# Performance work log

Hardware: AMD Instinct MI355X
Metric: run time of the kernel (lower is better)

The kernel has to match this reference:

```python
import jax, jax.numpy as jnp
import numpy as np

N_NODES = 100000
N_EDGES = 1600000
IN_CH = 128
OUT_CH = 64
HID = 2 * OUT_CH


def setup_inputs() -> dict:
    key = jax.random.key(0)
    ks = jax.random.split(key, 9)
    x = jax.random.normal(ks[0], (N_NODES, IN_CH), dtype=jnp.float32)
    edge_index = jax.random.randint(ks[1], (2, N_EDGES), 0, N_NODES, dtype=jnp.int64)
    s = 0.05
    W1 = jax.random.normal(ks[2], (IN_CH, HID), dtype=jnp.float32) * s
    b1 = jnp.zeros((HID,), dtype=jnp.float32)
    Wmu = jax.random.normal(ks[3], (HID, OUT_CH), dtype=jnp.float32) * s
    bmu = jnp.zeros((OUT_CH,), dtype=jnp.float32)
    Wls = jax.random.normal(ks[4], (HID, OUT_CH), dtype=jnp.float32) * s
    bls = jnp.zeros((OUT_CH,), dtype=jnp.float32)
    eps = jax.random.normal(ks[5], (N_NODES, OUT_CH), dtype=jnp.float32)
    return {"x": x, "edge_index": edge_index, "W1": W1, "b1": b1,
            "Wmu": Wmu, "bmu": bmu, "Wls": Wls, "bls": bls, "eps": eps}


def _gcn_conv(x, W, b, src, dst, dis):
    # PyG GCNConv: out = D^{-1/2}(A+I)D^{-1/2} X W + b, self-loops added.
    h = x @ W  # [N, F]
    norm = dis[src] * dis[dst]  # per-edge symmetric norm
    msg = h[src] * norm[:, None]  # [E, F] gathered + scaled messages
    agg = jax.ops.segment_sum(msg, dst, num_segments=x.shape[0])
    agg = agg + h * (dis * dis)[:, None]  # self-loop term
    return agg + b


def reference(x, edge_index, W1, b1, Wmu, bmu, Wls, bls, eps):
    src, dst = edge_index[0], edge_index[1]
    N = x.shape[0]
    # degree over A + I (aggregation at dst, +1 for self loop)
    deg = jax.ops.segment_sum(jnp.ones_like(dst, dtype=x.dtype), dst,
                              num_segments=N) + 1.0
    dis = jax.lax.rsqrt(deg)  # deg >= 1, safe
    h = _gcn_conv(x, W1, b1, src, dst, dis)
    mu = _gcn_conv(h, Wmu, bmu, src, dst, dis)
    logstd = _gcn_conv(h, Wls, bls, src, dst, dis)
    z = mu + eps * jnp.exp(logstd)  # reparametrization trick
    return (z, mu, logstd)
```

## Files before the change

kernel.cpp:

```cpp
#include <hip/hip_runtime.h>
#include <hip/hip_bf16.h>


typedef unsigned int u32;
typedef unsigned short u16;
typedef unsigned char u8;
typedef __bf16 bf16x8 __attribute__((ext_vector_type(8)));
typedef float f32x4 __attribute__((ext_vector_type(4)));

__device__ __forceinline__ u16 f2bf(float f) {
    union { float f; u32 u; } v; v.f = f;
    u32 u = v.u;
    u += 0x7fffu + ((u >> 16) & 1u);
    return (u16)(u >> 16);
}
__device__ __forceinline__ float bflo(u32 p) {
    union { u32 u; float f; } v; v.u = p << 16; return v.f;
}
__device__ __forceinline__ float bfhi(u32 p) {
    union { u32 u; float f; } v; v.u = p & 0xffff0000u; return v.f;
}

__global__ __launch_bounds__(256) void deg_hist(const int* __restrict__ dst,
                                                u32* __restrict__ deg,
                                                u8* __restrict__ loc, int E) {
    int i4 = (blockIdx.x * 256 + threadIdx.x) * 4;
    if (i4 + 3 < E) {
        int4 d4 = *(const int4*)(dst + i4);
        uchar4 l4;
        l4.x = (u8)atomicAdd(&deg[d4.x], 1u);
        l4.y = (u8)atomicAdd(&deg[d4.y], 1u);
        l4.z = (u8)atomicAdd(&deg[d4.z], 1u);
        l4.w = (u8)atomicAdd(&deg[d4.w], 1u);
        *(uchar4*)(loc + i4) = l4;
    } else {
        for (int i = i4; i < E; ++i) loc[i] = (u8)atomicAdd(&deg[dst[i]], 1u);
    }
}

__global__ __launch_bounds__(256) void scanA(const u32* __restrict__ deg,
                                             u32* __restrict__ blockSums, int N) {
    __shared__ u32 s[256];
    int t = threadIdx.x, i = blockIdx.x * 256 + t;
    s[t] = (i < N) ? deg[i] : 0u;
    for (int off = 128; off > 0; off >>= 1) {
        __syncthreads();
        if (t < off) s[t] += s[t + off];
    }
    if (t == 0) blockSums[blockIdx.x] = s[0];
}

__global__ __launch_bounds__(512) void scanB(const u32* __restrict__ blockSums,
                                             u32* __restrict__ blockOffs, int NB) {
    __shared__ u32 s[512];
    int t = threadIdx.x;
    u32 v = (t < NB) ? blockSums[t] : 0u;
    s[t] = v;
    for (int off = 1; off < 512; off <<= 1) {
        __syncthreads();
        u32 add = (t >= off) ? s[t - off] : 0u;
        __syncthreads();
        s[t] += add;
    }
    __syncthreads();
    if (t < NB) blockOffs[t] = s[t] - v;
}

__global__ __launch_bounds__(256) void scanC(const u32* __restrict__ deg,
                                             const u32* __restrict__ blockOffs,
                                             u32* __restrict__ rowstart,
                                             float* __restrict__ dis, int N, int E) {
    __shared__ u32 s[256];
    int t = threadIdx.x, i = blockIdx.x * 256 + t;
    u32 v = (i < N) ? deg[i] : 0u;
    s[t] = v;
    for (int off = 1; off < 256; off <<= 1) {
        __syncthreads();
        u32 add = (t >= off) ? s[t - off] : 0u;
        __syncthreads();
        s[t] += add;
    }
    __syncthreads();
    if (i < N) {
        rowstart[i] = blockOffs[blockIdx.x] + s[t] - v;
        dis[i] = rsqrtf((float)v + 1.0f);
    }
    if (i == 0) rowstart[N] = (u32)E;
}

__global__ __launch_bounds__(256) void place_kernel(const int* __restrict__ src,
                                                    const int* __restrict__ dst,
                                                    const u8* __restrict__ loc,
                                                    const u32* __restrict__ rowstart,
                                                    int* __restrict__ csr, int E) {
    int i4 = (blockIdx.x * 256 + threadIdx.x) * 4;
    if (i4 + 3 < E) {
        int4 s4 = *(const int4*)(src + i4);
        int4 d4 = *(const int4*)(dst + i4);
        uchar4 l4 = *(const uchar4*)(loc + i4);
        csr[rowstart[d4.x] + l4.x] = s4.x;
        csr[rowstart[d4.y] + l4.y] = s4.y;
        csr[rowstart[d4.z] + l4.z] = s4.z;
        csr[rowstart[d4.w] + l4.w] = s4.w;
    } else {
        for (int i = i4; i < E; ++i) csr[rowstart[dst[i]] + loc[i]] = src[i];
    }
}

__global__ __launch_bounds__(256) void fuse_w(const float* __restrict__ W1,
                                              const float* __restrict__ Wmu,
                                              const float* __restrict__ Wls,
                                              const float* __restrict__ b1,
                                              const float* __restrict__ bmu,
                                              const float* __restrict__ bls,
                                              u16* __restrict__ WfT,
                                              float* __restrict__ bb,
                                              float* __restrict__ bcat) {
    int idx = blockIdx.x * 256 + threadIdx.x;
    if (idx >= 16384) return;
    int k = idx >> 7, n = idx & 127;
    const float* Wcol = (n < 64) ? (Wmu + n) : (Wls + (n - 64));
    float acc = 0.f;
#pragma unroll 8
    for (int j = 0; j < 128; ++j) acc += W1[k * 128 + j] * Wcol[j * 64];
    WfT[n * 128 + k] = f2bf(acc);
    if (k == 0) {
        float accb = 0.f;
#pragma unroll 8
        for (int j = 0; j < 128; ++j) accb += b1[j] * Wcol[j * 64];
        bb[n] = accb;
        bcat[n] = (n < 64) ? bmu[n] : bls[n - 64];
    }
}

__global__ __launch_bounds__(256) void convert_x(const float* __restrict__ x,
                                                 const float* __restrict__ dis,
                                                 u32* __restrict__ xs,
                                                 u32* __restrict__ ts, int N) {
    long i = (long)blockIdx.x * 256 + threadIdx.x;
    long node = i >> 5;
    if (node > N) return;
    if (node == N) {
        ((uint2*)xs)[i] = make_uint2(0u, 0u);
        ((uint2*)ts)[i] = make_uint2(0u, 0u);
        return;
    }
    float dd = dis[node];
    f32x4 v = ((const f32x4*)x)[i];
    u32 p0 = (u32)f2bf(v[0] * dd) | ((u32)f2bf(v[1] * dd) << 16);
    u32 p1 = (u32)f2bf(v[2] * dd) | ((u32)f2bf(v[3] * dd) << 16);
    ((uint2*)xs)[i] = make_uint2(p0, p1);
}

__global__ __launch_bounds__(256) void g1gemm(const u32* __restrict__ xs,
                                              const int* __restrict__ csr,
                                              const u32* __restrict__ rowstart,
                                              const float* __restrict__ dis,
                                              const u16* __restrict__ WfT,
                                              const float* __restrict__ bb,
                                              u16* __restrict__ ts, int N) {
    __shared__ __align__(16) u16 ytile[16][136];
    __shared__ float disS[16];
    int tid = threadIdx.x, blk = blockIdx.x;
    int wave = tid >> 6, lane = tid & 63;
    int sub = lane >> 4, l = lane & 15;
    int nl = wave * 4 + sub;
    int node = blk * 16 + nl;
    bool live = node < N;
    int nodeC = live ? node : 0;
    float dd = dis[nodeC];
    u32 beg = live ? rowstart[nodeC] : 0u;
    u32 end = live ? rowstart[nodeC + 1] : 0u;
    if (tid < 16) disS[tid] = (blk * 16 + tid < N) ? dis[blk * 16 + tid] : 0.f;

    const uint4* xs4 = (const uint4*)xs;
    uint4 selfv = xs4[(long)nodeC * 16 + l];
    float a0 = bflo(selfv.x), a1 = bfhi(selfv.x);
    float a2 = bflo(selfv.y), a3 = bfhi(selfv.y);
    float a4 = bflo(selfv.z), a5 = bfhi(selfv.z);
    float a6 = bflo(selfv.w), a7 = bfhi(selfv.w);

    int s = (beg + (u32)l < end) ? csr[beg + l] : N;
    for (u32 e0 = beg; e0 < end; e0 += 16) {
        u32 e1 = e0 + 16;
        int sn = (e1 < end && e1 + (u32)l < end) ? csr[e1 + l] : N;
#pragma unroll
        for (int h = 0; h < 2; ++h) {
            int sj[8]; uint4 w[8];
#pragma unroll
            for (int j = 0; j < 8; ++j) sj[j] = __shfl(s, sub * 16 + h * 8 + j);
#pragma unroll
            for (int j = 0; j < 8; ++j) w[j] = xs4[(long)sj[j] * 16 + l];
#pragma unroll
            for (int j = 0; j < 8; ++j) {
                a0 += bflo(w[j].x); a1 += bfhi(w[j].x);
                a2 += bflo(w[j].y); a3 += bfhi(w[j].y);
                a4 += bflo(w[j].z); a5 += bfhi(w[j].z);
                a6 += bflo(w[j].w); a7 += bfhi(w[j].w);
            }
        }
        s = sn;
    }
    uint4 o = make_uint4(0u, 0u, 0u, 0u);
    if (live) {
        o.x = (u32)f2bf(a0 * dd) | ((u32)f2bf(a1 * dd) << 16);
        o.y = (u32)f2bf(a2 * dd) | ((u32)f2bf(a3 * dd) << 16);
        o.z = (u32)f2bf(a4 * dd) | ((u32)f2bf(a5 * dd) << 16);
        o.w = (u32)f2bf(a6 * dd) | ((u32)f2bf(a7 * dd) << 16);
    }
    *(uint4*)&ytile[nl][l * 8] = o;
    __syncthreads();

    int quad = sub, mn = l;
    bf16x8 af[4];
#pragma unroll
    for (int kk = 0; kk < 4; ++kk)
        af[kk] = *reinterpret_cast<const bf16x8*>(&ytile[mn][kk * 32 + quad * 8]);

#pragma unroll
    for (int n0 = 0; n0 < 2; ++n0) {
        int col = wave * 32 + n0 * 16 + mn;
        f32x4 acc = {0.f, 0.f, 0.f, 0.f};
#pragma unroll
        for (int kk = 0; kk < 4; ++kk) {
            bf16x8 bf =
                *reinterpret_cast<const bf16x8*>(&WfT[col * 128 + kk * 32 + quad * 8]);
            acc = __builtin_amdgcn_mfma_f32_16x16x32_bf16(af[kk], bf, acc, 0, 0, 0);
        }
        float bc = bb[col];
#pragma unroll
        for (int r = 0; r < 4; ++r) {
            int row = quad * 4 + r;
            int gn = blk * 16 + row;
            if (gn < N) ts[(long)gn * 128 + col] = f2bf((acc[r] + bc) * disS[row]);
        }
    }
}

__global__ __launch_bounds__(256) void gather2(const u32* __restrict__ ts,
                                               const int* __restrict__ csr,
                                               const u32* __restrict__ rowstart,
                                               const float* __restrict__ dis,
                                               const float* __restrict__ bcat,
                                               const float* __restrict__ eps,
                                               float* __restrict__ out, int N) {
    int wid = (blockIdx.x * 256 + threadIdx.x) >> 6;
    int sub = (threadIdx.x & 63) >> 4, l = threadIdx.x & 15;
    int node = wid * 4 + sub;
    bool live = node < N;
    int nodeC = live ? node : 0;
    float dd = dis[nodeC];
    u32 beg = live ? rowstart[nodeC] : 0u;
    u32 end = live ? rowstart[nodeC + 1] : 0u;
    const uint4* ts4 = (const uint4*)ts;

    uint4 selfv = ts4[(long)nodeC * 16 + l];
    float a0 = bflo(selfv.x), a1 = bfhi(selfv.x);
    float a2 = bflo(selfv.y), a3 = bfhi(selfv.y);
    float a4 = bflo(selfv.z), a5 = bfhi(selfv.z);
    float a6 = bflo(selfv.w), a7 = bfhi(selfv.w);

    int s = (beg + (u32)l < end) ? csr[beg + l] : N;
    for (u32 e0 = beg; e0 < end; e0 += 16) {
        u32 e1 = e0 + 16;
        int sn = (e1 < end && e1 + (u32)l < end) ? csr[e1 + l] : N;
#pragma unroll
        for (int h = 0; h < 2; ++h) {
            int sj[8]; uint4 w[8];
#pragma unroll
            for (int j = 0; j < 8; ++j) sj[j] = __shfl(s, sub * 16 + h * 8 + j);
#pragma unroll
            for (int j = 0; j < 8; ++j) w[j] = ts4[(long)sj[j] * 16 + l];
#pragma unroll
            for (int j = 0; j < 8; ++j) {
                a0 += bflo(w[j].x); a1 += bfhi(w[j].x);
                a2 += bflo(w[j].y); a3 += bfhi(w[j].y);
                a4 += bflo(w[j].z); a5 += bfhi(w[j].z);
                a6 += bflo(w[j].w); a7 += bfhi(w[j].w);
            }
        }
        s = sn;
    }

    int c0 = l * 8;
    f32x4 clo = ((const f32x4*)bcat)[2 * l], chi = ((const f32x4*)bcat)[2 * l + 1];
    float v0 = a0 * dd + clo[0];
    float v1 = a1 * dd + clo[1];
    float v2 = a2 * dd + clo[2];
    float v3 = a3 * dd + clo[3];
    float v4 = a4 * dd + chi[0];
    float v5 = a5 * dd + chi[1];
    float v6 = a6 * dd + chi[2];
    float v7 = a7 * dd + chi[3];

    int srcl = (threadIdx.x & 63) + 8;
    float w0 = __shfl(v0, srcl), w1 = __shfl(v1, srcl), w2 = __shfl(v2, srcl),
          w3 = __shfl(v3, srcl), w4 = __shfl(v4, srcl), w5 = __shfl(v5, srcl),
          w6 = __shfl(v6, srcl), w7 = __shfl(v7, srcl);

    if (!live) return;
    long NO = (long)N * 64;
    if (l < 8) {
        float* mu = out + NO + (long)node * 64 + c0;
        ((f32x4*)mu)[0] = f32x4{v0, v1, v2, v3};
        ((f32x4*)mu)[1] = f32x4{v4, v5, v6, v7};
        const float* ep = eps + (long)node * 64 + c0;
        f32x4 e0v = ((const f32x4*)ep)[0], e1v = ((const f32x4*)ep)[1];
        float* z = out + (long)node * 64 + c0;
        ((f32x4*)z)[0] = f32x4{v0 + e0v[0] * __expf(w0), v1 + e0v[1] * __expf(w1),
                               v2 + e0v[2] * __expf(w2), v3 + e0v[3] * __expf(w3)};
        ((f32x4*)z)[1] = f32x4{v4 + e1v[0] * __expf(w4), v5 + e1v[1] * __expf(w5),
                               v6 + e1v[2] * __expf(w6), v7 + e1v[3] * __expf(w7)};
    } else {
        float* ls = out + 2 * NO + (long)node * 64 + (c0 - 64);
        ((f32x4*)ls)[0] = f32x4{v0, v1, v2, v3};
        ((f32x4*)ls)[1] = f32x4{v4, v5, v6, v7};
    }
}

extern "C" void kernel_launch(void* const* d_in, const int* in_sizes, int n_in,
                              void* d_out, int out_size, void* d_ws, size_t ws_size,
                              hipStream_t stream) {
    const float* x   = (const float*)d_in[0];
    const int* ei    = (const int*)d_in[1];
    const float* W1  = (const float*)d_in[2];
    const float* b1  = (const float*)d_in[3];
    const float* Wmu = (const float*)d_in[4];
    const float* bmu = (const float*)d_in[5];
    const float* Wls = (const float*)d_in[6];
    const float* bls = (const float*)d_in[7];
    const float* eps = (const float*)d_in[8];
    float* out = (float*)d_out;

    const int N = in_sizes[0] / 128;
    const int E = in_sizes[1] / 2;
    const int* src = ei;
    const int* dst = ei + E;
    const int NB = (N + 255) / 256;

    char* ws = (char*)d_ws;
    u32* deg       = (u32*)(ws + 0);
    u32* rowstart  = (u32*)(ws + 401408);
    u32* blockSums = (u32*)(ws + 802816);
    u32* blockOffs = (u32*)(ws + 804864);
    float* dis     = (float*)(ws + 806912);
    u16* WfT       = (u16*)(ws + 1208320);
    float* bb      = (float*)(ws + 1241088);
    float* bcat    = (float*)(ws + 1241600);
    u8* loc        = (u8*)(ws + 1242112);
    int* csr       = (int*)(ws + 2842112);
    u32* xs        = (u32*)(ws + 9242112);
    u32* ts        = (u32*)(ws + 34842368);

    hipMemsetAsync(deg, 0, 400000, stream);

    int gridE4 = (E / 4 + 255) / 256;
    deg_hist<<<gridE4, 256, 0, stream>>>(dst, deg, loc, E);
    scanA<<<NB, 256, 0, stream>>>(deg, blockSums, N);
    scanB<<<1, 512, 0, stream>>>(blockSums, blockOffs, NB);
    scanC<<<NB, 256, 0, stream>>>(deg, blockOffs, rowstart, dis, N, E);
    place_kernel<<<gridE4, 256, 0, stream>>>(src, dst, loc, rowstart, csr, E);
    fuse_w<<<64, 256, 0, stream>>>(W1, Wmu, Wls, b1, bmu, bls, WfT, bb, bcat);

    long Qc = (long)(N + 1) * 32;
    convert_x<<<(int)((Qc + 255) / 256), 256, 0, stream>>>(x, dis, xs, ts, N);

    int gridT = (N + 15) / 16;
    g1gemm<<<gridT, 256, 0, stream>>>(xs, csr, rowstart, dis, WfT, bb,
                                      (u16*)ts, N);

    int gridG = ((N + 3) / 4 * 64 + 255) / 256;
    gather2<<<gridG, 256, 0, stream>>>(ts, csr, rowstart, dis, bcat, eps, out, N);
}
```

Measured before the change: 422.7 us.

## Slice feature tables into column panels and split gather from GEMM

The bf16 feature tables are stored as 8 column slices of 32 bytes per node. Each block now gathers one slice, so the random-access working set per slice is small enough to stay in cache. The fused gather+GEMM kernel is split into a separate gather pass that writes y and a standalone MFMA GEMM that writes the sliced layout, with non-temporal loads and stores for streaming data. The cost is an extra kernel launch, an extra round trip of y through memory, more redundant csr index reads (one per slice), and narrower per-lane gathers.

```diff
diff --git a/kernel.cpp b/kernel.cpp
--- a/kernel.cpp
+++ b/kernel.cpp
@@ -7,6 +7,8 @@
 typedef unsigned char u8;
 typedef __bf16 bf16x8 __attribute__((ext_vector_type(8)));
 typedef float f32x4 __attribute__((ext_vector_type(4)));
+typedef u32 u32x2 __attribute__((ext_vector_type(2)));
+typedef u32 u32x4 __attribute__((ext_vector_type(4)));
 
 __device__ __forceinline__ u16 f2bf(float f) {
     union { float f; u32 u; } v; v.f = f;
@@ -135,83 +137,124 @@
 
 __global__ __launch_bounds__(256) void convert_x(const float* __restrict__ x,
                                                  const float* __restrict__ dis,
-                                                 u32* __restrict__ xs,
-                                                 u32* __restrict__ ts, int N) {
+                                                 u32* __restrict__ xsP, int N) {
     long i = (long)blockIdx.x * 256 + threadIdx.x;
     long node = i >> 5;
+    int j = (int)(i & 31);
     if (node > N) return;
+    int s = j >> 2, q = j & 3;
+    u32x2* dst = (u32x2*)((char*)xsP + ((size_t)s * (N + 1) + node) * 32 + q * 8);
     if (node == N) {
-        ((uint2*)xs)[i] = make_uint2(0u, 0u);
-        ((uint2*)ts)[i] = make_uint2(0u, 0u);
+        u32x2 z = {0u, 0u};
+        __builtin_nontemporal_store(z, dst);
         return;
     }
     float dd = dis[node];
     f32x4 v = ((const f32x4*)x)[i];
-    u32 p0 = (u32)f2bf(v[0] * dd) | ((u32)f2bf(v[1] * dd) << 16);
-    u32 p1 = (u32)f2bf(v[2] * dd) | ((u32)f2bf(v[3] * dd) << 16);
-    ((uint2*)xs)[i] = make_uint2(p0, p1);
-}
-
-__global__ __launch_bounds__(256) void g1gemm(const u32* __restrict__ xs,
-                                              const int* __restrict__ csr,
-                                              const u32* __restrict__ rowstart,
-                                              const float* __restrict__ dis,
-                                              const u16* __restrict__ WfT,
-                                              const float* __restrict__ bb,
-                                              u16* __restrict__ ts, int N) {
-    __shared__ __align__(16) u16 ytile[16][136];
-    __shared__ float disS[16];
-    int tid = threadIdx.x, blk = blockIdx.x;
-    int wave = tid >> 6, lane = tid & 63;
-    int sub = lane >> 4, l = lane & 15;
-    int nl = wave * 4 + sub;
-    int node = blk * 16 + nl;
+    u32x2 o;
+    o.x = (u32)f2bf(v[0] * dd) | ((u32)f2bf(v[1] * dd) << 16);
+    o.y = (u32)f2bf(v[2] * dd) | ((u32)f2bf(v[3] * dd) << 16);
+    __builtin_nontemporal_store(o, dst);
+}
+
+#define GATHER_SLICE()                                                          \
+    int pairbase = (tid & 63) & ~1;                                             \
+    int id[8];                                                                  \
+    u32 e0 = beg;                                                               \
+    if (e0 < end) {                                                             \
+        _Pragma("unroll")                                                       \
+        for (int k = 0; k < 4; ++k) {                                           \
+            u32 q0 = e0 + p * 4 + k, q1 = e0 + 8 + p * 4 + k;                   \
+            id[k]     = (q0 < end) ? __builtin_nontemporal_load(csr + q0) : N;  \
+            id[4 + k] = (q1 < end) ? __builtin_nontemporal_load(csr + q1) : N;  \
+        }                                                                       \
+    }                                                                           \
+    for (; e0 < end;) {                                                         \
+        u32 e1 = e0 + 16;                                                       \
+        int idn[8];                                                             \
+        if (e1 < end) {                                                         \
+            _Pragma("unroll")                                                   \
+            for (int k = 0; k < 4; ++k) {                                       \
+                u32 q0 = e1 + p * 4 + k, q1 = e1 + 8 + p * 4 + k;               \
+                idn[k]     = (q0 < end) ? __builtin_nontemporal_load(csr + q0) : N; \
+                idn[4 + k] = (q1 < end) ? __builtin_nontemporal_load(csr + q1) : N; \
+            }                                                                   \
+        }                                                                       \
+        _Pragma("unroll")                                                       \
+        for (int h = 0; h < 2; ++h) {                                           \
+            int sj[8]; uint4 w[8];                                              \
+            _Pragma("unroll")                                                   \
+            for (int j = 0; j < 8; ++j)                                         \
+                sj[j] = __shfl(id[h * 4 + (j & 3)], pairbase + (j >> 2));       \
+            _Pragma("unroll")                                                   \
+            for (int j = 0; j < 8; ++j) w[j] = base[(size_t)sj[j] * 2];         \
+            _Pragma("unroll")                                                   \
+            for (int j = 0; j < 8; ++j) {                                       \
+                a0 += bflo(w[j].x); a1 += bfhi(w[j].x);                         \
+                a2 += bflo(w[j].y); a3 += bfhi(w[j].y);                         \
+                a4 += bflo(w[j].z); a5 += bfhi(w[j].z);                         \
+                a6 += bflo(w[j].w); a7 += bfhi(w[j].w);                         \
+            }                                                                   \
+        }                                                                       \
+        _Pragma("unroll")                                                       \
+        for (int k = 0; k < 8; ++k) id[k] = idn[k];                             \
+        e0 = e1;                                                                \
+    }
+
+__global__ __launch_bounds__(256) void gatherY(const u32* __restrict__ xsP,
+                                               const int* __restrict__ csr,
+                                               const u32* __restrict__ rowstart,
+                                               const float* __restrict__ dis,
+                                               u16* __restrict__ y, int N) {
+    int tid = threadIdx.x;
+    u32 bid = blockIdx.x;
+    int s = bid & 7;
+    int p = tid & 1;
+    int node = (int)(bid >> 3) * 128 + (tid >> 1);
     bool live = node < N;
     int nodeC = live ? node : 0;
     float dd = dis[nodeC];
-    u32 beg = live ? rowstart[nodeC] : 0u;
-    u32 end = live ? rowstart[nodeC + 1] : 0u;
-    if (tid < 16) disS[tid] = (blk * 16 + tid < N) ? dis[blk * 16 + tid] : 0.f;
-
-    const uint4* xs4 = (const uint4*)xs;
-    uint4 selfv = xs4[(long)nodeC * 16 + l];
+    u32 beg = rowstart[nodeC];
+    u32 end = live ? rowstart[nodeC + 1] : beg;
+    const uint4* base = (const uint4*)(xsP + (size_t)s * (N + 1) * 8) + p;
+
+    uint4 selfv = base[(size_t)nodeC * 2];
     float a0 = bflo(selfv.x), a1 = bfhi(selfv.x);
     float a2 = bflo(selfv.y), a3 = bfhi(selfv.y);
     float a4 = bflo(selfv.z), a5 = bfhi(selfv.z);
     float a6 = bflo(selfv.w), a7 = bfhi(selfv.w);
 
-    int s = (beg + (u32)l < end) ? csr[beg + l] : N;
-    for (u32 e0 = beg; e0 < end; e0 += 16) {
-        u32 e1 = e0 + 16;
-        int sn = (e1 < end && e1 + (u32)l < end) ? csr[e1 + l] : N;
-#pragma unroll
-        for (int h = 0; h < 2; ++h) {
-            int sj[8]; uint4 w[8];
-#pragma unroll
-            for (int j = 0; j < 8; ++j) sj[j] = __shfl(s, sub * 16 + h * 8 + j);
-#pragma unroll
-            for (int j = 0; j < 8; ++j) w[j] = xs4[(long)sj[j] * 16 + l];
-#pragma unroll
-            for (int j = 0; j < 8; ++j) {
-                a0 += bflo(w[j].x); a1 += bfhi(w[j].x);
-                a2 += bflo(w[j].y); a3 += bfhi(w[j].y);
-                a4 += bflo(w[j].z); a5 += bfhi(w[j].z);
-                a6 += bflo(w[j].w); a7 += bfhi(w[j].w);
-            }
-        }
-        s = sn;
-    }
-    uint4 o = make_uint4(0u, 0u, 0u, 0u);
+    GATHER_SLICE()
+
     if (live) {
+        u32x4 o;
         o.x = (u32)f2bf(a0 * dd) | ((u32)f2bf(a1 * dd) << 16);
         o.y = (u32)f2bf(a2 * dd) | ((u32)f2bf(a3 * dd) << 16);
         o.z = (u32)f2bf(a4 * dd) | ((u32)f2bf(a5 * dd) << 16);
         o.w = (u32)f2bf(a6 * dd) | ((u32)f2bf(a7 * dd) << 16);
-    }
-    *(uint4*)&ytile[nl][l * 8] = o;
+        u32x4* dst = (u32x4*)(y + (size_t)node * 128 + s * 16 + p * 8);
+        __builtin_nontemporal_store(o, dst);
+    }
+}
+
+__global__ __launch_bounds__(256) void gemm1(const u16* __restrict__ y,
+                                             const u16* __restrict__ WfT,
+                                             const float* __restrict__ bb,
+                                             const float* __restrict__ dis,
+                                             u16* __restrict__ tsP, int N) {
+    __shared__ __align__(16) u16 ytile[16][136];
+    __shared__ float disS[16];
+    int tid = threadIdx.x, blk = blockIdx.x;
+    int node0 = blk * 16;
+    if (tid < 16) disS[tid] = (node0 + tid < N) ? dis[node0 + tid] : 0.f;
+    int row = tid >> 4, ch = tid & 15;
+    int gn = node0 + row;
+    int gnC = (gn < N) ? gn : (N - 1);
+    uint4 av = ((const uint4*)y)[(size_t)gnC * 16 + ch];
+    *(uint4*)&ytile[row][ch * 8] = av;
     __syncthreads();
 
-    int quad = sub, mn = l;
+    int wave = tid >> 6, lane = tid & 63, quad = lane >> 4, mn = lane & 15;
     bf16x8 af[4];
 #pragma unroll
     for (int kk = 0; kk < 4; ++kk)
@@ -228,93 +271,78 @@
             acc = __builtin_amdgcn_mfma_f32_16x16x32_bf16(af[kk], bf, acc, 0, 0, 0);
         }
         float bc = bb[col];
+        int sC = (col < 64) ? (col >> 3) : ((col - 64) >> 3);
+        int posC = (col & 7) + ((col < 64) ? 0 : 8);
+        u16* op = tsP + ((size_t)sC * (N + 1) + node0) * 16 + posC;
 #pragma unroll
         for (int r = 0; r < 4; ++r) {
-            int row = quad * 4 + r;
-            int gn = blk * 16 + row;
-            if (gn < N) ts[(long)gn * 128 + col] = f2bf((acc[r] + bc) * disS[row]);
+            int rr = quad * 4 + r;
+            if (node0 + rr < N)
+                __builtin_nontemporal_store(f2bf((acc[r] + bc) * disS[rr]),
+                                            op + (size_t)rr * 16);
         }
     }
 }
 
-__global__ __launch_bounds__(256) void gather2(const u32* __restrict__ ts,
+__global__ __launch_bounds__(256) void gatherZ(const u32* __restrict__ tsP,
                                                const int* __restrict__ csr,
                                                const u32* __restrict__ rowstart,
                                                const float* __restrict__ dis,
                                                const float* __restrict__ bcat,
                                                const float* __restrict__ eps,
                                                float* __restrict__ out, int N) {
-    int wid = (blockIdx.x * 256 + threadIdx.x) >> 6;
-    int sub = (threadIdx.x & 63) >> 4, l = threadIdx.x & 15;
-    int node = wid * 4 + sub;
+    int tid = threadIdx.x;
+    u32 bid = blockIdx.x;
+    int s = bid & 7;
+    int p = tid & 1;
+    int node = (int)(bid >> 3) * 128 + (tid >> 1);
     bool live = node < N;
     int nodeC = live ? node : 0;
     float dd = dis[nodeC];
-    u32 beg = live ? rowstart[nodeC] : 0u;
-    u32 end = live ? rowstart[nodeC + 1] : 0u;
-    const uint4* ts4 = (const uint4*)ts;
-
-    uint4 selfv = ts4[(long)nodeC * 16 + l];
+    u32 beg = rowstart[nodeC];
+    u32 end = live ? rowstart[nodeC + 1] : beg;
+    const uint4* base = (const uint4*)(tsP + (size_t)s * (N + 1) * 8) + p;
+
+    uint4 selfv = base[(size_t)nodeC * 2];
     float a0 = bflo(selfv.x), a1 = bfhi(selfv.x);
     float a2 = bflo(selfv.y), a3 = bfhi(selfv.y);
     float a4 = bflo(selfv.z), a5 = bfhi(selfv.z);
     float a6 = bflo(selfv.w), a7 = bfhi(selfv.w);
 
-    int s = (beg + (u32)l < end) ? csr[beg + l] : N;
-    for (u32 e0 = beg; e0 < end; e0 += 16) {
-        u32 e1 = e0 + 16;
-        int sn = (e1 < end && e1 + (u32)l < end) ? csr[e1 + l] : N;
-#pragma unroll
-        for (int h = 0; h < 2; ++h) {
-            int sj[8]; uint4 w[8];
-#pragma unroll
-            for (int j = 0; j < 8; ++j) sj[j] = __shfl(s, sub * 16 + h * 8 + j);
-#pragma unroll
-            for (int j = 0; j < 8; ++j) w[j] = ts4[(long)sj[j] * 16 + l];
-#pragma unroll
-            for (int j = 0; j < 8; ++j) {
-                a0 += bflo(w[j].x); a1 += bfhi(w[j].x);
-                a2 += bflo(w[j].y); a3 += bfhi(w[j].y);
-                a4 += bflo(w[j].z); a5 += bfhi(w[j].z);
-                a6 += bflo(w[j].w); a7 += bfhi(w[j].w);
-            }
-        }
-        s = sn;
-    }
-
-    int c0 = l * 8;
-    f32x4 clo = ((const f32x4*)bcat)[2 * l], chi = ((const f32x4*)bcat)[2 * l + 1];
-    float v0 = a0 * dd + clo[0];
-    float v1 = a1 * dd + clo[1];
-    float v2 = a2 * dd + clo[2];
-    float v3 = a3 * dd + clo[3];
-    float v4 = a4 * dd + chi[0];
-    float v5 = a5 * dd + chi[1];
-    float v6 = a6 * dd + chi[2];
-    float v7 = a7 * dd + chi[3];
-
-    int srcl = (threadIdx.x & 63) + 8;
-    float w0 = __shfl(v0, srcl), w1 = __shfl(v1, srcl), w2 = __shfl(v2, srcl),
-          w3 = __shfl(v3, srcl), w4 = __shfl(v4, srcl), w5 = __shfl(v5, srcl),
-          w6 = __shfl(v6, srcl), w7 = __shfl(v7, srcl);
+    GATHER_SLICE()
+
+    const f32x4* bc = (const f32x4*)(bcat + (p ? 64 + 8 * s : 8 * s));
+    f32x4 c0 = bc[0], c1 = bc[1];
+    float v0 = a0 * dd + c0[0], v1 = a1 * dd + c0[1];
+    float v2 = a2 * dd + c0[2], v3 = a3 * dd + c0[3];
+    float v4 = a4 * dd + c1[0], v5 = a5 * dd + c1[1];
+    float v6 = a6 * dd + c1[2], v7 = a7 * dd + c1[3];
+
+    int lsrc = (tid & 63) | 1;
+    float w0 = __shfl(v0, lsrc), w1 = __shfl(v1, lsrc), w2 = __shfl(v2, lsrc),
+          w3 = __shfl(v3, lsrc), w4 = __shfl(v4, lsrc), w5 = __shfl(v5, lsrc),
+          w6 = __shfl(v6, lsrc), w7 = __shfl(v7, lsrc);
 
     if (!live) return;
     long NO = (long)N * 64;
-    if (l < 8) {
-        float* mu = out + NO + (long)node * 64 + c0;
-        ((f32x4*)mu)[0] = f32x4{v0, v1, v2, v3};
-        ((f32x4*)mu)[1] = f32x4{v4, v5, v6, v7};
-        const float* ep = eps + (long)node * 64 + c0;
-        f32x4 e0v = ((const f32x4*)ep)[0], e1v = ((const f32x4*)ep)[1];
-        float* z = out + (long)node * 64 + c0;
-        ((f32x4*)z)[0] = f32x4{v0 + e0v[0] * __expf(w0), v1 + e0v[1] * __expf(w1),
-                               v2 + e0v[2] * __expf(w2), v3 + e0v[3] * __expf(w3)};
-        ((f32x4*)z)[1] = f32x4{v4 + e1v[0] * __expf(w4), v5 + e1v[1] * __expf(w5),
-                               v6 + e1v[2] * __expf(w6), v7 + e1v[3] * __expf(w7)};
+    if (p == 0) {
+        float* mu = out + NO + (long)node * 64 + 8 * s;
+        __builtin_nontemporal_store(f32x4{v0, v1, v2, v3}, (f32x4*)mu);
+        __builtin_nontemporal_store(f32x4{v4, v5, v6, v7}, (f32x4*)mu + 1);
+        const f32x4* ep = (const f32x4*)(eps + (long)node * 64 + 8 * s);
+        f32x4 e0v = __builtin_nontemporal_load(ep);
+        f32x4 e1v = __builtin_nontemporal_load(ep + 1);
+        float* z = out + (long)node * 64 + 8 * s;
+        f32x4 z0 = {v0 + e0v[0] * __expf(w0), v1 + e0v[1] * __expf(w1),
+                    v2 + e0v[2] * __expf(w2), v3 + e0v[3] * __expf(w3)};
+        f32x4 z1 = {v4 + e1v[0] * __expf(w4), v5 + e1v[1] * __expf(w5),
+                    v6 + e1v[2] * __expf(w6), v7 + e1v[3] * __expf(w7)};
+        __builtin_nontemporal_store(z0, (f32x4*)z);
+        __builtin_nontemporal_store(z1, (f32x4*)z + 1);
     } else {
-        float* ls = out + 2 * NO + (long)node * 64 + (c0 - 64);
-        ((f32x4*)ls)[0] = f32x4{v0, v1, v2, v3};
-        ((f32x4*)ls)[1] = f32x4{v4, v5, v6, v7};
+        float* ls = out + 2 * NO + (long)node * 64 + 8 * s;
+        __builtin_nontemporal_store(f32x4{v0, v1, v2, v3}, (f32x4*)ls);
+        __builtin_nontemporal_store(f32x4{v4, v5, v6, v7}, (f32x4*)ls + 1);
     }
 }
 
@@ -349,8 +377,9 @@
     float* bcat    = (float*)(ws + 1241600);
     u8* loc        = (u8*)(ws + 1242112);
     int* csr       = (int*)(ws + 2842112);
-    u32* xs        = (u32*)(ws + 9242112);
-    u32* ts        = (u32*)(ws + 34842368);
+    u32* xsP       = (u32*)(ws + 9242112);
+    u16* y         = (u16*)(ws + 34842368);
+    u16* tsP       = (u16*)xsP;
 
     hipMemsetAsync(deg, 0, 400000, stream);
 
@@ -363,12 +392,13 @@
     fuse_w<<<64, 256, 0, stream>>>(W1, Wmu, Wls, b1, bmu, bls, WfT, bb, bcat);
 
     long Qc = (long)(N + 1) * 32;
-    convert_x<<<(int)((Qc + 255) / 256), 256, 0, stream>>>(x, dis, xs, ts, N);
-
-    int gridT = (N + 15) / 16;
-    g1gemm<<<gridT, 256, 0, stream>>>(xs, csr, rowstart, dis, WfT, bb,
-                                      (u16*)ts, N);
-
-    int gridG = ((N + 3) / 4 * 64 + 255) / 256;
-    gather2<<<gridG, 256, 0, stream>>>(ts, csr, rowstart, dis, bcat, eps, out, N);
-}
+    convert_x<<<(int)((Qc + 255) / 256), 256, 0, stream>>>(x, dis, xsP, N);
+
+    int gridS = 8 * ((N + 127) / 128);
+    gatherY<<<gridS, 256, 0, stream>>>(xsP, csr, rowstart, dis, y, N);
+
+    gemm1<<<(N + 15) / 16, 256, 0, stream>>>(y, WfT, bb, dis, tsP, N);
+
+    gatherZ<<<gridS, 256, 0, stream>>>((const u32*)tsP, csr, rowstart, dis,
+                                       bcat, eps, out, N);
+}
```

Result: slower. 643.8 us (+52.3%).
